# Kernel optimization log

Hardware: AMD Instinct MI355X
Metric: run time of the kernel (lower is better)

Reference implementation:

```python
import jax, jax.numpy as jnp
import numpy as np

B, C, H, W = 4, 256, 48, 48
OUT = 256


def conv1x1(x, w, b):
    # 1x1 conv == per-pixel linear: x [B,Cin,H,W], w [Cout,Cin], b [Cout]
    return jnp.einsum('bchw,oc->bohw', x, w) + b[None, :, None, None]


def setup_inputs() -> dict:
    key = jax.random.key(0)
    ks = jax.random.split(key, 40)
    std = 1.0 / np.sqrt(C)
    inp = {
        'x0': jax.random.normal(ks[0], (B, C, H, W), jnp.float32),
        'x1': jax.random.normal(ks[1], (B, C, H, W), jnp.float32),
        'x2': jax.random.normal(ks[2], (B, C, H, W), jnp.float32),
        's': jax.random.uniform(ks[3], (3,), jnp.float32),
    }
    names = ['wq0', 'wk0', 'wv0', 'wq1', 'wk1', 'wv1', 'wq2', 'wk2', 'wv2', 'wg']
    for i, n in enumerate(names):
        inp[n] = jax.random.normal(ks[4 + 2 * i], (C, C), jnp.float32) * std
        inp['b' + n[1:]] = jax.random.normal(ks[5 + 2 * i], (C,), jnp.float32) * 0.01
    inp['wo'] = jax.random.normal(ks[36], (OUT, C), jnp.float32) * std
    inp['bo'] = jax.random.normal(ks[37], (OUT,), jnp.float32) * 0.01
    return inp


def reference(x0, x1, x2, s,
              wq0, bq0, wk0, bk0, wv0, bv0,
              wq1, bq1, wk1, bk1, wv1, bv1,
              wq2, bq2, wk2, bk2, wv2, bv2,
              wg, bg, wo, bo):
    # rgb=x0 (scale s[0]), thermal=x1 (s[1]), depth=x2 (s[2])
    qr = conv1x1(x0, wq0, bq0) * s[0]
    kr = conv1x1(x0, wk0, bk0) * s[0]
    vr = conv1x1(x0, wv0, bv0)
    qt = conv1x1(x1, wq1, bq1) * s[1]
    kt = conv1x1(x1, wk1, bk1) * s[1]
    vt = conv1x1(x1, wv1, bv1)
    qd = conv1x1(x2, wq2, bq2) * s[2]
    kd = conv1x1(x2, wk2, bk2) * s[2]
    vd = conv1x1(x2, wv2, bv2)

    fl = lambda t: t.reshape(B, C, H * W)  # [B,C,N]
    scale = jnp.sqrt(jnp.float32(C))

    def attend(q, ka, kb, v):
        # q^T@ka + q^T@kb == q^T@(ka+kb): [B,N,N] scores
        scores = jnp.einsum('bcn,bcm->bnm', fl(q), fl(ka) + fl(kb)) / scale
        a = jax.nn.softmax(scores, axis=-1)
        return jnp.einsum('bnm,bcm->bcn', a, fl(v)).reshape(B, C, H, W)

    w_rgb = attend(qr, kd, kt, vr)
    w_depth = attend(qd, kr, kt, vd)
    w_thermal = attend(qt, kr, kd, vt)

    gate = lambda t: jax.nn.sigmoid(conv1x1(t, wg, bg)) * t
    fused = gate(w_rgb) + gate(w_depth) + gate(w_thermal)
    return conv1x1(fused, wo, bo)
```

## Files before the change

### kernel.cpp

```cpp
#include <hip/hip_runtime.h>
#include <cstdint>
#include <cstddef>

#define DEVINL __device__ __forceinline__

typedef __attribute__((ext_vector_type(8))) short short8v;
typedef __attribute__((ext_vector_type(4))) float f32x4;

static constexpr int CB   = 4;
static constexpr int CC   = 256;
static constexpr int NN   = 2304;
static constexpr int RALL = CB * NN;

DEVINL uint16_t f2b(float f) {
    uint32_t u = __builtin_bit_cast(uint32_t, f);
    u = (u + 0x7FFFu + ((u >> 16) & 1u)) >> 16;
    return (uint16_t)u;
}
DEVINL float b2f(uint16_t u) {
    return __builtin_bit_cast(float, (uint32_t)u << 16);
}

__global__ __launch_bounds__(1024)
void transpose_k(const float* __restrict__ x0, const float* __restrict__ x1,
                 const float* __restrict__ x2, uint16_t* __restrict__ Xt) {
    int mod = blockIdx.z >> 2;
    int b   = blockIdx.z & 3;
    const float* x = (mod == 0) ? x0 : ((mod == 1) ? x1 : x2);
    __shared__ float tile[32][33];
    int n0 = blockIdx.x * 32, c0 = blockIdx.y * 32;
    int tx = threadIdx.x, ty = threadIdx.y;
    tile[ty][tx] = x[((size_t)b * CC + c0 + ty) * NN + n0 + tx];
    __syncthreads();
    float v = tile[tx][ty];
    Xt[(size_t)mod * RALL * CC + ((size_t)b * NN + n0 + ty) * CC + c0 + tx] = f2b(v);
}

struct PackPtrs { const float* w[11]; const float* bsrc[11]; };

__global__ __launch_bounds__(256)
void pack_k(PackPtrs pp, uint16_t* __restrict__ Wbf, float* __restrict__ Bpk) {
    int j = blockIdx.y;
    if (blockIdx.x == 32) {
        Bpk[j * 256 + threadIdx.x] = pp.bsrc[j][threadIdx.x];
    } else {
        int base = blockIdx.x * 2048 + threadIdx.x * 8;
        const float* src = pp.w[j] + base;
        uint16_t* dst = Wbf + (size_t)j * 65536 + base;
        #pragma unroll
        for (int i = 0; i < 8; i++) dst[i] = f2b(src[i]);
    }
}

__global__ __launch_bounds__(256)
void ksum_k(const uint16_t* __restrict__ Kt, uint16_t* __restrict__ Ks) {
    int a = blockIdx.y;
    int m1 = (a == 0) ? 2 : 0;
    int m2 = (a == 2) ? 2 : 1;
    size_t idx = ((size_t)blockIdx.x * 256 + threadIdx.x) * 4;
    const uint16_t* p1 = Kt + (size_t)m1 * RALL * CC + idx;
    const uint16_t* p2 = Kt + (size_t)m2 * RALL * CC + idx;
    uint16_t* pd = Ks + (size_t)a * RALL * CC + idx;
    #pragma unroll
    for (int i = 0; i < 4; i++) pd[i] = f2b(b2f(p1[i]) + b2f(p2[i]));
}

__global__ __launch_bounds__(256)
void fuse_k(const uint16_t* __restrict__ gated, uint16_t* __restrict__ fused) {
    size_t idx = ((size_t)blockIdx.x * 256 + threadIdx.x) * 4;
    #pragma unroll
    for (int i = 0; i < 4; i++) {
        float v = b2f(gated[idx + i])
                + b2f(gated[(size_t)RALL * CC + idx + i])
                + b2f(gated[(size_t)2 * RALL * CC + idx + i]);
        fused[idx + i] = f2b(v);
    }
}

enum Modes { MQK = 0, MV = 1, MSC = 2, MPV = 3, MG = 4, MF = 5 };

struct GemmArgs {
    const uint16_t* A; const uint16_t* B; void* D;
    long Az, Bz, Dz;
    int lda, ldb, ldd, K;
    const float* bias; long biasz;
    const uint16_t* extra; long extraz;
    const float* sdev; float smul;
    float* rsum;
    int p0;
};

template<int MODE>
__global__ __launch_bounds__(256)
void gemm_k(GemmArgs p) {
    __shared__ __align__(16) uint8_t As[128 * 128];
    __shared__ __align__(16) uint8_t Bs[128 * 128];

    const int t  = threadIdx.x;
    const int l  = t & 63;
    const int w  = t >> 6;
    const int wr = w >> 1;
    const int wc = w & 1;
    const int z  = blockIdx.z;

    const uint16_t* Aab;
    const uint16_t* Bb;
    uint16_t* Dbf = nullptr;
    float*    Df  = nullptr;
    const float* bias = nullptr;
    const uint16_t* extra = nullptr;
    float* rsum = nullptr;

    if constexpr (MODE == MSC || MODE == MPV) {
        int pp = p.p0 + z;
        int a = pp >> 2, b = pp & 3;
        int qm = (a == 0) ? 0 : ((a == 1) ? 2 : 1);
        rsum = p.rsum + (size_t)z * NN;
        if constexpr (MODE == MSC) {
            Aab = p.A + (size_t)qm * RALL * CC + (size_t)b * NN * CC;
            Bb  = p.B + (size_t)a  * RALL * CC + (size_t)b * NN * CC;
            Dbf = (uint16_t*)p.D + (size_t)z * NN * NN;
        } else {
            Aab = p.A + (size_t)z * NN * NN;
            Bb  = p.B + (size_t)qm * CB * CC * NN + (size_t)b * CC * NN;
            Dbf = (uint16_t*)p.D + (size_t)a * RALL * CC + (size_t)b * NN * CC;
        }
    } else {
        Aab = p.A + (size_t)z * p.Az;
        Bb  = p.B + (size_t)z * p.Bz;
        if constexpr (MODE == MF) Df = (float*)p.D + (size_t)z * p.Dz;
        else                      Dbf = (uint16_t*)p.D + (size_t)z * p.Dz;
        if (p.bias) bias = p.bias + (size_t)z * p.biasz;
        if constexpr (MODE == MG) extra = p.extra + (size_t)z * p.extraz;
    }

    const int lda = p.lda, ldb = p.ldb, ldd = p.ldd;
    const long tR = (long)blockIdx.x * 128;
    const long tC = (long)blockIdx.y * 128;

    const int swz = ((l & 7) ^ ((l >> 3) & 7)) * 8;
    const uint16_t* sA = Aab + (size_t)(tR + w * 32 + (l >> 3)) * lda + swz;
    const uint16_t* sB = Bb  + (size_t)(tC + w * 32 + (l >> 3)) * ldb + swz;

    auto* As3 = (__attribute__((address_space(3))) uint8_t*)As;
    auto* Bs3 = (__attribute__((address_space(3))) uint8_t*)Bs;

    f32x4 acc[4][4];
    #pragma unroll
    for (int i = 0; i < 4; i++)
        #pragma unroll
        for (int j = 0; j < 4; j++) {
            f32x4 zz = {0.f, 0.f, 0.f, 0.f};
            acc[i][j] = zz;
        }

    const int nk = p.K >> 6;
    for (int kt = 0; kt < nk; ++kt) {
        #pragma unroll
        for (int q = 0; q < 4; q++) {
            __builtin_amdgcn_global_load_lds(
                (__attribute__((address_space(1))) void*)(sA + (size_t)q * 8 * lda),
                (__attribute__((address_space(3))) void*)(As3 + w * 4096 + q * 1024),
                16, 0, 0);
            __builtin_amdgcn_global_load_lds(
                (__attribute__((address_space(1))) void*)(sB + (size_t)q * 8 * ldb),
                (__attribute__((address_space(3))) void*)(Bs3 + w * 4096 + q * 1024),
                16, 0, 0);
        }
        sA += 64; sB += 64;
        __syncthreads();

        #pragma unroll
        for (int kk = 0; kk < 2; kk++) {
            short8v af[4], bfv[4];
            #pragma unroll
            for (int i = 0; i < 4; i++) {
                int rowA = wr * 64 + i * 16 + (l & 15);
                int offA = rowA * 128 + ((kk * 64 + ((l >> 4) << 4)) ^ ((rowA & 7) << 4));
                af[i] = *(const short8v*)(As + offA);
                int rowB = wc * 64 + i * 16 + (l & 15);
                int offB = rowB * 128 + ((kk * 64 + ((l >> 4) << 4)) ^ ((rowB & 7) << 4));
                bfv[i] = *(const short8v*)(Bs + offB);
            }
            #pragma unroll
            for (int i = 0; i < 4; i++)
                #pragma unroll
                for (int j = 0; j < 4; j++)
                    acc[i][j] = __builtin_amdgcn_mfma_f32_16x16x32_bf16(
                        af[i], bfv[j], acc[i][j], 0, 0, 0);
        }
        __syncthreads();
    }

    float scale = 1.0f;
    if constexpr (MODE == MQK) scale = p.sdev[z] * p.smul;

    const int rq = (l >> 4) << 2;
    const int cq = l & 15;
    #pragma unroll
    for (int i = 0; i < 4; i++) {
        #pragma unroll
        for (int r4 = 0; r4 < 4; r4++) {
            long row = tR + wr * 64 + i * 16 + rq + r4;
            if constexpr (MODE == MSC) {
                float part = 0.f;
                #pragma unroll
                for (int j = 0; j < 4; j++) {
                    long col = tC + wc * 64 + j * 16 + cq;
                    float e = __expf(acc[i][j][r4]);
                    part += e;
                    Dbf[row * ldd + col] = f2b(e);
                }
                part += __shfl_xor(part, 1);
                part += __shfl_xor(part, 2);
                part += __shfl_xor(part, 4);
                part += __shfl_xor(part, 8);
                if ((l & 15) == 0) atomicAdd(&rsum[row], part);
            } else if constexpr (MODE == MPV) {
                float inv = 1.0f / rsum[row];
                #pragma unroll
                for (int j = 0; j < 4; j++) {
                    long col = tC + wc * 64 + j * 16 + cq;
                    Dbf[row * ldd + col] = f2b(acc[i][j][r4] * inv);
                }
            } else {
                #pragma unroll
                for (int j = 0; j < 4; j++) {
                    long col = tC + wc * 64 + j * 16 + cq;
                    float v = acc[i][j][r4];
                    if constexpr (MODE == MQK) {
                        Dbf[row * ldd + col] = f2b((v + bias[col]) * scale);
                    } else if constexpr (MODE == MV) {
                        Dbf[row * ldd + col] = f2b(v + bias[row]);
                    } else if constexpr (MODE == MG) {
                        float g = v + bias[col];
                        float sig = 1.0f / (1.0f + __expf(-g));
                        Dbf[row * ldd + col] = f2b(sig * b2f(extra[row * ldd + col]));
                    } else {
                        Df[row * ldd + col] = v + bias[row];
                    }
                }
            }
        }
    }
}

extern "C" void kernel_launch(void* const* d_in, const int* in_sizes, int n_in,
                              void* d_out, int out_size, void* d_ws, size_t ws_size,
                              hipStream_t stream) {
    const float* x0   = (const float*)d_in[0];
    const float* x1   = (const float*)d_in[1];
    const float* x2   = (const float*)d_in[2];
    const float* sdev = (const float*)d_in[3];

    uint8_t* ws = (uint8_t*)d_ws;
    const size_t off_W  = 0;
    const size_t off_Bp = 1441792;
    const size_t off_Xt = 1453312;
    const size_t TEN    = (size_t)3 * RALL * CC * 2;
    const size_t off_Qt = off_Xt + TEN;
    const size_t off_Kt = off_Qt + TEN;
    const size_t off_Ks = off_Kt + TEN;
    const size_t off_V  = off_Ks + TEN;
    const size_t off_R  = off_V + TEN;
    const size_t off_S  = off_R + (size_t)12 * NN * 4;
    const size_t s_pair = (size_t)NN * NN * 2;

    uint16_t* Wbf = (uint16_t*)(ws + off_W);
    float*    Bpk = (float*)(ws + off_Bp);
    uint16_t* Xt  = (uint16_t*)(ws + off_Xt);
    uint16_t* Qt  = (uint16_t*)(ws + off_Qt);
    uint16_t* Kt  = (uint16_t*)(ws + off_Kt);
    uint16_t* Ks  = (uint16_t*)(ws + off_Ks);
    uint16_t* V   = (uint16_t*)(ws + off_V);
    float*    Rs  = (float*)(ws + off_R);
    uint16_t* Ot    = Xt;
    uint16_t* gated = Kt;
    uint16_t* fused = Ks;
    float* out = (float*)d_out;

    size_t fit = (ws_size > off_S) ? (ws_size - off_S) / s_pair : 0;
    int g = (int)(fit > 12 ? 12 : fit);
    uint16_t* S = (g >= 1) ? (uint16_t*)(ws + off_S) : Kt;
    if (g < 1) g = 1;

    transpose_k<<<dim3(72, 8, 12), dim3(32, 32), 0, stream>>>(x0, x1, x2, Xt);

    PackPtrs pp;
    const int wIdx[11] = {4, 6, 8, 10, 12, 14, 16, 18, 20, 22, 24};
    for (int j = 0; j < 11; j++) {
        pp.w[j]    = (const float*)d_in[wIdx[j]];
        pp.bsrc[j] = (const float*)d_in[wIdx[j] + 1];
    }
    pack_k<<<dim3(33, 11), 256, 0, stream>>>(pp, Wbf, Bpk);

    {
        GemmArgs a{};
        a.A = Xt;  a.Az = (long)RALL * CC; a.lda = CC;
        a.B = Wbf; a.Bz = 3 * 65536;       a.ldb = CC;
        a.D = Qt;  a.Dz = (long)RALL * CC; a.ldd = CC;
        a.K = CC; a.bias = Bpk; a.biasz = 3 * 256;
        a.sdev = sdev; a.smul = 0.0625f;
        gemm_k<MQK><<<dim3(72, 2, 3), 256, 0, stream>>>(a);
        a.B = Wbf + 65536; a.D = Kt; a.bias = Bpk + 256; a.smul = 1.0f;
        gemm_k<MQK><<<dim3(72, 2, 3), 256, 0, stream>>>(a);
    }

    for (int m = 0; m < 3; m++) {
        GemmArgs a{};
        a.A = Wbf + (size_t)(2 + 3 * m) * 65536; a.Az = 0;              a.lda = CC;
        a.B = Xt + (size_t)m * RALL * CC;        a.Bz = (long)NN * CC;  a.ldb = CC;
        a.D = V + (size_t)m * CB * CC * NN;      a.Dz = (long)CC * NN;  a.ldd = NN;
        a.K = CC; a.bias = Bpk + (2 + 3 * m) * 256; a.biasz = 0;
        gemm_k<MV><<<dim3(2, 18, 4), 256, 0, stream>>>(a);
    }

    ksum_k<<<dim3(2304, 3), 256, 0, stream>>>(Kt, Ks);

    for (int p0 = 0; p0 < 12; p0 += g) {
        int gc = (12 - p0 < g) ? (12 - p0) : g;
        hipMemsetAsync(Rs, 0, (size_t)gc * NN * 4, stream);

        GemmArgs sc{};
        sc.A = Qt; sc.B = Ks; sc.D = S; sc.p0 = p0; sc.rsum = Rs;
        sc.lda = CC; sc.ldb = CC; sc.ldd = NN; sc.K = CC;
        gemm_k<MSC><<<dim3(18, 18, gc), 256, 0, stream>>>(sc);

        GemmArgs pv{};
        pv.A = S; pv.B = V; pv.D = Ot; pv.p0 = p0; pv.rsum = Rs;
        pv.lda = NN; pv.ldb = NN; pv.ldd = CC; pv.K = NN;
        gemm_k<MPV><<<dim3(18, 2, gc), 256, 0, stream>>>(pv);
    }

    {
        GemmArgs a{};
        a.A = Ot;    a.Az = (long)RALL * CC; a.lda = CC;
        a.B = Wbf + (size_t)9 * 65536; a.Bz = 0; a.ldb = CC;
        a.D = gated; a.Dz = (long)RALL * CC; a.ldd = CC;
        a.K = CC; a.bias = Bpk + 9 * 256; a.biasz = 0;
        a.extra = Ot; a.extraz = (long)RALL * CC;
        gemm_k<MG><<<dim3(72, 2, 3), 256, 0, stream>>>(a);
    }

    fuse_k<<<dim3(2304), 256, 0, stream>>>(gated, fused);

    {
        GemmArgs a{};
        a.A = Wbf + (size_t)10 * 65536; a.Az = 0; a.lda = CC;
        a.B = fused; a.Bz = (long)NN * CC; a.ldb = CC;
        a.D = out;   a.Dz = (long)CC * NN; a.ldd = NN;
        a.K = CC; a.bias = Bpk + 10 * 256; a.biasz = 0;
        gemm_k<MF><<<dim3(2, 18, 4), 256, 0, stream>>>(a);
    }
}
```

Measured before the change: 360.6 us.

## Add dedicated score kernel, double-buffer GEMM tiles, merge projection launches

Replaces the generic score GEMM with a dedicated kernel. Each block keeps a 128-row Q tile resident in LDS, streams double-buffered K tiles across the full row, and reduces row sums in-block instead of using atomics. This removes the memset and the atomicAdd traffic. The generic GEMM gains double-buffered LDS loads so global loads overlap MFMA work. The Q/K projection launches are merged into one grid, and the three V projection launches into another, to cut launch count. The score kernel uses 128KB of LDS per block, which limits occupancy to one block per CU.

```diff
diff --git a/kernel.cpp b/kernel.cpp
--- a/kernel.cpp
+++ b/kernel.cpp
@@ -3,6 +3,9 @@
 #include <cstddef>
 
 #define DEVINL __device__ __forceinline__
+#define AS1 __attribute__((address_space(1)))
+#define AS3 __attribute__((address_space(3)))
+#define GLOAD16(src, dst) __builtin_amdgcn_global_load_lds((AS1 void*)(src), (AS3 void*)(dst), 16, 0, 0)
 
 typedef __attribute__((ext_vector_type(8))) short short8v;
 typedef __attribute__((ext_vector_type(4))) float f32x4;
@@ -77,24 +80,144 @@
     }
 }
 
-enum Modes { MQK = 0, MV = 1, MSC = 2, MPV = 3, MG = 4, MF = 5 };
+__global__ __launch_bounds__(512)
+void msc_k(const uint16_t* __restrict__ Qt, const uint16_t* __restrict__ Ksg,
+           uint16_t* __restrict__ S, float* __restrict__ Rs, int p0) {
+    __shared__ __align__(16) uint8_t Qs[65536];
+    __shared__ __align__(16) uint8_t Kb[65536];
+
+    const int t = threadIdx.x, l = t & 63, w = t >> 6;
+    const int wr = w >> 1, wc = w & 1;
+    const int z = blockIdx.z;
+    const int pp = p0 + z;
+    const int a = pp >> 2, b = pp & 3;
+    const int qm = (a == 0) ? 0 : ((a == 1) ? 2 : 1);
+
+    const uint16_t* Qb = Qt + (size_t)qm * RALL * CC + (size_t)b * NN * CC
+                            + (size_t)blockIdx.x * 128 * CC;
+    const uint16_t* Kg = Ksg + (size_t)a * RALL * CC + (size_t)b * NN * CC;
+    uint16_t* Sg = S + (size_t)z * NN * NN + (size_t)blockIdx.x * 128 * NN;
+    float*    Rg = Rs + (size_t)z * NN + blockIdx.x * 128;
+
+    auto* QsL = (AS3 uint8_t*)Qs;
+    auto* KbL = (AS3 uint8_t*)Kb;
+
+    {
+        #pragma unroll
+        for (int st = 0; st < 4; ++st)
+            #pragma unroll
+            for (int it = 0; it < 2; ++it) {
+                int o = it * 8192 + t * 16;
+                int row = o >> 7, slot = (o >> 4) & 7;
+                GLOAD16(Qb + (size_t)row * CC + st * 64 + (slot ^ (row & 7)) * 8,
+                        QsL + st * 16384 + o);
+            }
+        int row = t >> 3, slot = t & 7;
+        #pragma unroll
+        for (int st = 0; st < 4; ++st)
+            GLOAD16(Kg + (size_t)row * CC + st * 64 + (slot ^ (row & 7)) * 8,
+                    KbL + st * 8192 + t * 16);
+    }
+    __syncthreads();
+
+    float rsum[2][4];
+    #pragma unroll
+    for (int i = 0; i < 2; ++i)
+        #pragma unroll
+        for (int r4 = 0; r4 < 4; ++r4) rsum[i][r4] = 0.f;
+
+    int cbuf = 0;
+    for (int mt = 0; mt < 36; ++mt) {
+        if (mt + 1 < 36) {
+            int row = t >> 3, slot = t & 7;
+            #pragma unroll
+            for (int st = 0; st < 4; ++st)
+                GLOAD16(Kg + (size_t)(mt + 1) * 64 * CC + (size_t)row * CC
+                           + st * 64 + (slot ^ (row & 7)) * 8,
+                        KbL + (cbuf ^ 1) * 32768 + st * 8192 + t * 16);
+        }
+        f32x4 acc2[2][2];
+        #pragma unroll
+        for (int i = 0; i < 2; ++i)
+            #pragma unroll
+            for (int j = 0; j < 2; ++j) {
+                f32x4 zz = {0.f, 0.f, 0.f, 0.f};
+                acc2[i][j] = zz;
+            }
+        #pragma unroll
+        for (int ks = 0; ks < 8; ++ks) {
+            int st = ks >> 1, kk = ks & 1;
+            short8v qa[2], kb2[2];
+            #pragma unroll
+            for (int i = 0; i < 2; ++i) {
+                int rowA = wr * 32 + i * 16 + (l & 15);
+                qa[i] = *(const short8v*)(Qs + st * 16384 + rowA * 128
+                          + ((kk * 64 + (l >> 4) * 16) ^ ((rowA & 7) << 4)));
+                int rowB = wc * 32 + i * 16 + (l & 15);
+                kb2[i] = *(const short8v*)(Kb + cbuf * 32768 + st * 8192 + rowB * 128
+                          + ((kk * 64 + (l >> 4) * 16) ^ ((rowB & 7) << 4)));
+            }
+            #pragma unroll
+            for (int i = 0; i < 2; ++i)
+                #pragma unroll
+                for (int j = 0; j < 2; ++j)
+                    acc2[i][j] = __builtin_amdgcn_mfma_f32_16x16x32_bf16(
+                        qa[i], kb2[j], acc2[i][j], 0, 0, 0);
+        }
+        {
+            int rq = (l >> 4) << 2, cq = l & 15;
+            #pragma unroll
+            for (int i = 0; i < 2; ++i)
+                #pragma unroll
+                for (int r4 = 0; r4 < 4; ++r4) {
+                    int rl = wr * 32 + i * 16 + rq + r4;
+                    #pragma unroll
+                    for (int j = 0; j < 2; ++j) {
+                        float e = __expf(acc2[i][j][r4]);
+                        rsum[i][r4] += e;
+                        Sg[(size_t)rl * NN + mt * 64 + wc * 32 + j * 16 + cq] = f2b(e);
+                    }
+                }
+        }
+        __syncthreads();
+        cbuf ^= 1;
+    }
+
+    float* red = (float*)Qs;
+    {
+        int rq = (l >> 4) << 2;
+        #pragma unroll
+        for (int i = 0; i < 2; ++i)
+            #pragma unroll
+            for (int r4 = 0; r4 < 4; ++r4) {
+                float v = rsum[i][r4];
+                v += __shfl_xor(v, 1); v += __shfl_xor(v, 2);
+                v += __shfl_xor(v, 4); v += __shfl_xor(v, 8);
+                if ((l & 15) == 0) red[(wr * 32 + i * 16 + rq + r4) * 2 + wc] = v;
+            }
+    }
+    __syncthreads();
+    if (t < 128) Rg[t] = red[t * 2] + red[t * 2 + 1];
+}
+
+enum Modes { MQK = 0, MV = 1, MPV = 3, MG = 4, MF = 5 };
 
 struct GemmArgs {
-    const uint16_t* A; const uint16_t* B; void* D;
+    const uint16_t* A; const uint16_t* B; void* D; void* D2;
     long Az, Bz, Dz;
     int lda, ldb, ldd, K;
-    const float* bias; long biasz;
+    const float* bias;
     const uint16_t* extra; long extraz;
-    const float* sdev; float smul;
-    float* rsum;
+    const float* sdev;
+    const float* rsum;
     int p0;
 };
 
 template<int MODE>
 __global__ __launch_bounds__(256)
 void gemm_k(GemmArgs p) {
-    __shared__ __align__(16) uint8_t As[128 * 128];
-    __shared__ __align__(16) uint8_t Bs[128 * 128];
+    __shared__ __align__(16) uint8_t As[32768];
+    __shared__ __align__(16) uint8_t Bs[32768];
 
     const int t  = threadIdx.x;
     const int l  = t & 63;
@@ -109,28 +232,36 @@
     float*    Df  = nullptr;
     const float* bias = nullptr;
     const uint16_t* extra = nullptr;
-    float* rsum = nullptr;
-
-    if constexpr (MODE == MSC || MODE == MPV) {
+    const float* rsum = nullptr;
+    float scale = 1.0f;
+
+    if constexpr (MODE == MPV) {
         int pp = p.p0 + z;
         int a = pp >> 2, b = pp & 3;
         int qm = (a == 0) ? 0 : ((a == 1) ? 2 : 1);
         rsum = p.rsum + (size_t)z * NN;
-        if constexpr (MODE == MSC) {
-            Aab = p.A + (size_t)qm * RALL * CC + (size_t)b * NN * CC;
-            Bb  = p.B + (size_t)a  * RALL * CC + (size_t)b * NN * CC;
-            Dbf = (uint16_t*)p.D + (size_t)z * NN * NN;
-        } else {
-            Aab = p.A + (size_t)z * NN * NN;
-            Bb  = p.B + (size_t)qm * CB * CC * NN + (size_t)b * CC * NN;
-            Dbf = (uint16_t*)p.D + (size_t)a * RALL * CC + (size_t)b * NN * CC;
-        }
+        Aab = p.A + (size_t)z * NN * NN;
+        Bb  = p.B + (size_t)qm * CB * CC * NN + (size_t)b * CC * NN;
+        Dbf = (uint16_t*)p.D + (size_t)a * RALL * CC + (size_t)b * NN * CC;
+    } else if constexpr (MODE == MQK) {
+        int mod = z % 3, qk = z / 3;
+        Aab = p.A + (size_t)mod * p.Az;
+        Bb  = p.B + (size_t)(mod * 3 + qk) * 65536;
+        Dbf = (uint16_t*)(qk ? p.D2 : p.D) + (size_t)mod * p.Dz;
+        bias = p.bias + (size_t)(mod * 3 + qk) * 256;
+        scale = p.sdev[mod] * (qk ? 1.0f : 0.0625f);
+    } else if constexpr (MODE == MV) {
+        int mod = z >> 2, bb = z & 3;
+        Aab = p.A + (size_t)(2 + 3 * mod) * 65536;
+        Bb  = p.B + (size_t)mod * RALL * CC + (size_t)bb * NN * CC;
+        Dbf = (uint16_t*)p.D + (size_t)mod * CB * CC * NN + (size_t)bb * CC * NN;
+        bias = p.bias + (size_t)(2 + 3 * mod) * 256;
     } else {
         Aab = p.A + (size_t)z * p.Az;
         Bb  = p.B + (size_t)z * p.Bz;
         if constexpr (MODE == MF) Df = (float*)p.D + (size_t)z * p.Dz;
         else                      Dbf = (uint16_t*)p.D + (size_t)z * p.Dz;
-        if (p.bias) bias = p.bias + (size_t)z * p.biasz;
+        if (p.bias) bias = p.bias;
         if constexpr (MODE == MG) extra = p.extra + (size_t)z * p.extraz;
     }
 
@@ -142,8 +273,8 @@
     const uint16_t* sA = Aab + (size_t)(tR + w * 32 + (l >> 3)) * lda + swz;
     const uint16_t* sB = Bb  + (size_t)(tC + w * 32 + (l >> 3)) * ldb + swz;
 
-    auto* As3 = (__attribute__((address_space(3))) uint8_t*)As;
-    auto* Bs3 = (__attribute__((address_space(3))) uint8_t*)Bs;
+    auto* As3 = (AS3 uint8_t*)As;
+    auto* Bs3 = (AS3 uint8_t*)Bs;
 
     f32x4 acc[4][4];
     #pragma unroll
@@ -155,31 +286,36 @@
         }
 
     const int nk = p.K >> 6;
+    #pragma unroll
+    for (int q = 0; q < 4; q++) {
+        GLOAD16(sA + (size_t)q * 8 * lda, As3 + w * 4096 + q * 1024);
+        GLOAD16(sB + (size_t)q * 8 * ldb, Bs3 + w * 4096 + q * 1024);
+    }
+    __syncthreads();
+
     for (int kt = 0; kt < nk; ++kt) {
-        #pragma unroll
-        for (int q = 0; q < 4; q++) {
-            __builtin_amdgcn_global_load_lds(
-                (__attribute__((address_space(1))) void*)(sA + (size_t)q * 8 * lda),
-                (__attribute__((address_space(3))) void*)(As3 + w * 4096 + q * 1024),
-                16, 0, 0);
-            __builtin_amdgcn_global_load_lds(
-                (__attribute__((address_space(1))) void*)(sB + (size_t)q * 8 * ldb),
-                (__attribute__((address_space(3))) void*)(Bs3 + w * 4096 + q * 1024),
-                16, 0, 0);
-        }
-        sA += 64; sB += 64;
-        __syncthreads();
-
+        const int cb = kt & 1;
+        if (kt + 1 < nk) {
+            #pragma unroll
+            for (int q = 0; q < 4; q++) {
+                GLOAD16(sA + (size_t)(kt + 1) * 64 + (size_t)q * 8 * lda,
+                        As3 + (cb ^ 1) * 16384 + w * 4096 + q * 1024);
+                GLOAD16(sB + (size_t)(kt + 1) * 64 + (size_t)q * 8 * ldb,
+                        Bs3 + (cb ^ 1) * 16384 + w * 4096 + q * 1024);
+            }
+        }
         #pragma unroll
         for (int kk = 0; kk < 2; kk++) {
             short8v af[4], bfv[4];
             #pragma unroll
             for (int i = 0; i < 4; i++) {
                 int rowA = wr * 64 + i * 16 + (l & 15);
-                int offA = rowA * 128 + ((kk * 64 + ((l >> 4) << 4)) ^ ((rowA & 7) << 4));
+                int offA = cb * 16384 + rowA * 128
+                         + ((kk * 64 + ((l >> 4) << 4)) ^ ((rowA & 7) << 4));
                 af[i] = *(const short8v*)(As + offA);
                 int rowB = wc * 64 + i * 16 + (l & 15);
-                int offB = rowB * 128 + ((kk * 64 + ((l >> 4) << 4)) ^ ((rowB & 7) << 4));
+                int offB = cb * 16384 + rowB * 128
+                         + ((kk * 64 + ((l >> 4) << 4)) ^ ((rowB & 7) << 4));
                 bfv[i] = *(const short8v*)(Bs + offB);
             }
             #pragma unroll
@@ -192,9 +328,6 @@
         __syncthreads();
     }
 
-    float scale = 1.0f;
-    if constexpr (MODE == MQK) scale = p.sdev[z] * p.smul;
-
     const int rq = (l >> 4) << 2;
     const int cq = l & 15;
     #pragma unroll
@@ -202,21 +335,7 @@
         #pragma unroll
         for (int r4 = 0; r4 < 4; r4++) {
             long row = tR + wr * 64 + i * 16 + rq + r4;
-            if constexpr (MODE == MSC) {
-                float part = 0.f;
-                #pragma unroll
-                for (int j = 0; j < 4; j++) {
-                    long col = tC + wc * 64 + j * 16 + cq;
-                    float e = __expf(acc[i][j][r4]);
-                    part += e;
-                    Dbf[row * ldd + col] = f2b(e);
-                }
-                part += __shfl_xor(part, 1);
-                part += __shfl_xor(part, 2);
-                part += __shfl_xor(part, 4);
-                part += __shfl_xor(part, 8);
-                if ((l & 15) == 0) atomicAdd(&rsum[row], part);
-            } else if constexpr (MODE == MPV) {
+            if constexpr (MODE == MPV) {
                 float inv = 1.0f / rsum[row];
                 #pragma unroll
                 for (int j = 0; j < 4; j++) {
@@ -297,34 +416,27 @@
     {
         GemmArgs a{};
         a.A = Xt;  a.Az = (long)RALL * CC; a.lda = CC;
-        a.B = Wbf; a.Bz = 3 * 65536;       a.ldb = CC;
-        a.D = Qt;  a.Dz = (long)RALL * CC; a.ldd = CC;
-        a.K = CC; a.bias = Bpk; a.biasz = 3 * 256;
-        a.sdev = sdev; a.smul = 0.0625f;
-        gemm_k<MQK><<<dim3(72, 2, 3), 256, 0, stream>>>(a);
-        a.B = Wbf + 65536; a.D = Kt; a.bias = Bpk + 256; a.smul = 1.0f;
-        gemm_k<MQK><<<dim3(72, 2, 3), 256, 0, stream>>>(a);
-    }
-
-    for (int m = 0; m < 3; m++) {
+        a.B = Wbf; a.ldb = CC;
+        a.D = Qt;  a.D2 = Kt; a.Dz = (long)RALL * CC; a.ldd = CC;
+        a.K = CC; a.bias = Bpk; a.sdev = sdev;
+        gemm_k<MQK><<<dim3(72, 2, 6), 256, 0, stream>>>(a);
+    }
+
+    {
         GemmArgs a{};
-        a.A = Wbf + (size_t)(2 + 3 * m) * 65536; a.Az = 0;              a.lda = CC;
-        a.B = Xt + (size_t)m * RALL * CC;        a.Bz = (long)NN * CC;  a.ldb = CC;
-        a.D = V + (size_t)m * CB * CC * NN;      a.Dz = (long)CC * NN;  a.ldd = NN;
-        a.K = CC; a.bias = Bpk + (2 + 3 * m) * 256; a.biasz = 0;
-        gemm_k<MV><<<dim3(2, 18, 4), 256, 0, stream>>>(a);
+        a.A = Wbf; a.lda = CC;
+        a.B = Xt;  a.ldb = CC;
+        a.D = V;   a.ldd = NN;
+        a.K = CC; a.bias = Bpk;
+        gemm_k<MV><<<dim3(2, 18, 12), 256, 0, stream>>>(a);
     }
 
     ksum_k<<<dim3(2304, 3), 256, 0, stream>>>(Kt, Ks);
 
     for (int p0 = 0; p0 < 12; p0 += g) {
         int gc = (12 - p0 < g) ? (12 - p0) : g;
-        hipMemsetAsync(Rs, 0, (size_t)gc * NN * 4, stream);
-
-        GemmArgs sc{};
-        sc.A = Qt; sc.B = Ks; sc.D = S; sc.p0 = p0; sc.rsum = Rs;
-        sc.lda = CC; sc.ldb = CC; sc.ldd = NN; sc.K = CC;
-        gemm_k<MSC><<<dim3(18, 18, gc), 256, 0, stream>>>(sc);
+
+        msc_k<<<dim3(18, 1, gc), 512, 0, stream>>>(Qt, Ks, S, Rs, p0);
 
         GemmArgs pv{};
         pv.A = S; pv.B = V; pv.D = Ot; pv.p0 = p0; pv.rsum = Rs;
@@ -337,7 +449,7 @@
         a.A = Ot;    a.Az = (long)RALL * CC; a.lda = CC;
         a.B = Wbf + (size_t)9 * 65536; a.Bz = 0; a.ldb = CC;
         a.D = gated; a.Dz = (long)RALL * CC; a.ldd = CC;
-        a.K = CC; a.bias = Bpk + 9 * 256; a.biasz = 0;
+        a.K = CC; a.bias = Bpk + 9 * 256;
         a.extra = Ot; a.extraz = (long)RALL * CC;
         gemm_k<MG><<<dim3(72, 2, 3), 256, 0, stream>>>(a);
     }
@@ -349,7 +461,7 @@
         a.A = Wbf + (size_t)10 * 65536; a.Az = 0; a.lda = CC;
         a.B = fused; a.Bz = (long)NN * CC; a.ldb = CC;
         a.D = out;   a.Dz = (long)CC * NN; a.ldd = NN;
-        a.K = CC; a.bias = Bpk + 10 * 256; a.biasz = 0;
+        a.K = CC; a.bias = Bpk + 10 * 256;
         gemm_k<MF><<<dim3(2, 18, 4), 256, 0, stream>>>(a);
     }
 }
```

Measured after the change: 317.9 us. -11.8%, faster.
